# Optimization experiments

Measured on AMD Instinct MI355X. Metric: run time of the kernel, lower is better.

Reference implementation:

```python
import jax, jax.numpy as jnp
import numpy as np

N_EMBD = 512
Q_N_EMBD = 512
N_HEAD = 8
EPS = 1e-5


def _layernorm(x, w, b):
    mu = jnp.mean(x, axis=-1, keepdims=True)
    var = jnp.mean(jnp.square(x - mu), axis=-1, keepdims=True)
    return (x - mu) * jax.lax.rsqrt(var + EPS) * w + b


def setup_inputs() -> dict:
    key = jax.random.key(0)
    ks = jax.random.split(key, 16)
    B, C, H, W = 8, N_EMBD, 32, 32
    s = 1.0 / np.sqrt(N_EMBD)
    inp = {
        "q": jax.random.normal(ks[0], (B, Q_N_EMBD, H, W), jnp.float32),
        "kv": jax.random.normal(ks[1], (B, C, H, W), jnp.float32),
        "ln_kv_w": jnp.ones((N_EMBD,), jnp.float32),
        "ln_kv_b": jnp.zeros((N_EMBD,), jnp.float32),
        "ln_q_w": jnp.ones((Q_N_EMBD,), jnp.float32),
        "ln_q_b": jnp.zeros((Q_N_EMBD,), jnp.float32),
        "Wk": jax.random.normal(ks[2], (N_EMBD, N_EMBD), jnp.float32) * s,
        "bk": jnp.zeros((N_EMBD,), jnp.float32),
        "Wq": jax.random.normal(ks[3], (Q_N_EMBD, N_EMBD), jnp.float32) * s,
        "bq": jnp.zeros((N_EMBD,), jnp.float32),
        "Wv": jax.random.normal(ks[4], (N_EMBD, N_EMBD), jnp.float32) * s,
        "bv": jnp.zeros((N_EMBD,), jnp.float32),
        "Wp": jax.random.normal(ks[5], (N_EMBD, N_EMBD), jnp.float32) * s,
        "bp": jnp.zeros((N_EMBD,), jnp.float32),
    }
    return inp


def reference(q, kv, ln_kv_w, ln_kv_b, ln_q_w, ln_q_b,
              Wk, bk, Wq, bq, Wv, bv, Wp, bp):
    B, C, H, W = kv.shape
    c_q = q.shape[1]
    T = H * W
    hd = C // N_HEAD  # head dim

    # [B, C, H, W] -> [B, T, C] tokens
    kv_t = kv.reshape(B, C, T).transpose(0, 2, 1)
    q_t = q.reshape(B, c_q, T).transpose(0, 2, 1)

    kv_n = _layernorm(kv_t, ln_kv_w, ln_kv_b)
    q_n = _layernorm(q_t, ln_q_w, ln_q_b)

    # projections, split heads: [B, T, C] -> [B, H, T, hd]
    def heads(x):
        return x.reshape(B, T, N_HEAD, hd).transpose(0, 2, 1, 3)

    k = heads(kv_n @ Wk + bk)
    qh = heads(q_n @ Wq + bq)
    v = heads(kv_n @ Wv + bv)

    att = jnp.einsum('bhqd,bhkd->bhqk', qh, k) * (1.0 / np.sqrt(hd))
    att = jax.nn.softmax(att, axis=-1)
    y = jnp.einsum('bhqk,bhkd->bhqd', att, v)
    y = y.transpose(0, 2, 1, 3).reshape(B, T, C)
    y = y @ Wp + bp

    x = kv_t + y  # residual on (pre-LN) kv tokens
    return x.transpose(0, 2, 1).reshape(B, C, H, W)
```

## Files before the change

kernel.cpp:

```cpp
#include <hip/hip_runtime.h>
#include <stdint.h>

#define DI static __device__ __forceinline__

typedef __attribute__((ext_vector_type(8))) short bh8;
typedef __attribute__((ext_vector_type(4))) float f4;

DI short f2bf(float f) {
  unsigned u = __float_as_uint(f);
  u += 0x7fffu + ((u >> 16) & 1u);
  return (short)(u >> 16);
}

DI unsigned pkbf(float a, float b) {
  unsigned ua = __float_as_uint(a) + 0x8000u;
  unsigned ub = __float_as_uint(b) + 0x8000u;
  return __builtin_amdgcn_perm(ub, ua, 0x07060302u);
}

DI unsigned pk4fp8(float a, float b, float c, float d) {
  unsigned w = 0;
  w = __builtin_amdgcn_cvt_pk_fp8_f32(a, b, w, false);
  w = __builtin_amdgcn_cvt_pk_fp8_f32(c, d, w, true);
  return w;
}

DI void gll16(const void* g, void* l) {
  __builtin_amdgcn_global_load_lds(
      (const __attribute__((address_space(1))) unsigned int*)g,
      (__attribute__((address_space(3))) unsigned int*)l, 16, 0, 0);
}

DI f4 mfma16(bh8 a, bh8 b, f4 c) {
  return __builtin_amdgcn_mfma_f32_16x16x32_bf16(a, b, c, 0, 0, 0);
}

DI f4 mfma8(long a, long b, f4 c) {
  return __builtin_amdgcn_mfma_f32_16x16x32_fp8_fp8(a, b, c, 0, 0, 0);
}

DI bh8 ld8(const short* p) { return *(const bh8*)p; }

__global__ __launch_bounds__(256) void prep_k(
    const float* __restrict__ kv, const float* __restrict__ qi,
    const float* __restrict__ kw, const float* __restrict__ kbv,
    const float* __restrict__ qw, const float* __restrict__ qbv,
    const float* __restrict__ Wk, const float* __restrict__ Wq,
    const float* __restrict__ Wv, const float* __restrict__ Wp,
    short* __restrict__ kvn, short* __restrict__ qn,
    short* __restrict__ Wt)
{
  __shared__ char sm[16 * 516 * 4 + 128];
  int role = blockIdx.y;
  int bx = blockIdx.x;
  int tid = threadIdx.x;

  if (role < 4) {
    if (bx >= 256) return;
    float (*ts)[33] = (float(*)[33])sm;
    const float* w = (role == 0) ? Wk : (role == 1) ? Wq : (role == 2) ? Wv : Wp;
    short* o = Wt + ((size_t)role << 18);
    int c0 = (bx & 15) << 5, r0 = (bx >> 4) << 5;
    int tx = tid & 31, ty = tid >> 5;
#pragma unroll
    for (int k = 0; k < 32; k += 8)
      ts[ty + k][tx] = w[((size_t)(r0 + ty + k) << 9) + c0 + tx];
    __syncthreads();
#pragma unroll
    for (int k = 0; k < 32; k += 8)
      o[((size_t)(c0 + ty + k) << 9) + r0 + tx] = f2bf(ts[tx][ty + k]);
    return;
  }

  float (*xs)[516] = (float(*)[516])sm;
  float* smean = (float*)(sm + 16 * 516 * 4);
  float* srstd = smean + 16;
  int which = role - 4;
  const float* x = which ? qi : kv;
  const float* w = which ? qw : kw;
  const float* bb = which ? qbv : kbv;
  short* o = which ? qn : kvn;
  int b = bx >> 6;
  int t0 = (bx & 63) << 4;
  const float* xb = x + ((size_t)b << 19) + (size_t)t0;
#pragma unroll
  for (int k = 0; k < 8; k++) {
    int idx = (k << 8) + tid;
    int c = idx >> 2, tt = (idx & 3) << 2;
    float4 v = *(const float4*)(xb + ((size_t)c << 10) + tt);
    xs[tt + 0][c] = v.x; xs[tt + 1][c] = v.y;
    xs[tt + 2][c] = v.z; xs[tt + 3][c] = v.w;
  }
  __syncthreads();
  {
    int t = tid >> 4, cp = tid & 15;
    float s = 0.f, s2 = 0.f;
#pragma unroll
    for (int k = 0; k < 8; k++) {
      float4 v = *(const float4*)&xs[t][(cp << 2) + (k << 6)];
      s  += v.x + v.y + v.z + v.w;
      s2 += v.x * v.x + v.y * v.y + v.z * v.z + v.w * v.w;
    }
#pragma unroll
    for (int m = 1; m < 16; m <<= 1) {
      s  += __shfl_xor(s,  m);
      s2 += __shfl_xor(s2, m);
    }
    if (cp == 0) {
      float mean = s * (1.f / 512.f);
      float var  = s2 * (1.f / 512.f) - mean * mean;
      smean[t] = mean;
      srstd[t] = rsqrtf(var + 1e-5f);
    }
  }
  __syncthreads();
#pragma unroll
  for (int k = 0; k < 8; k++) {
    int idx = (k << 8) + tid;
    int t = idx >> 7, c = (idx & 127) << 2;
    float4 v = *(const float4*)&xs[t][c];
    float4 wv = *(const float4*)(w + c);
    float4 bv4 = *(const float4*)(bb + c);
    float mu = smean[t], rs = srstd[t];
    float r0 = (v.x - mu) * rs * wv.x + bv4.x;
    float r1 = (v.y - mu) * rs * wv.y + bv4.y;
    float r2 = (v.z - mu) * rs * wv.z + bv4.z;
    float r3 = (v.w - mu) * rs * wv.w + bv4.w;
    uint2 pk; pk.x = pkbf(r0, r1); pk.y = pkbf(r2, r3);
    *(uint2*)(o + (((size_t)(b << 10) + t0 + t) << 9) + c) = pk;
  }
}

__global__ __launch_bounds__(256, 3) void gemm_qkv_k(
    const short* __restrict__ kvn, const short* __restrict__ qn,
    const short* __restrict__ Wt,
    const float* __restrict__ bk, const float* __restrict__ bq,
    const float* __restrict__ bv,
    unsigned char* __restrict__ kb8, unsigned char* __restrict__ qb8,
    unsigned char* __restrict__ vb8)
{
  __shared__ short As[128 * 64];
  __shared__ short Bs[128 * 64];
  int z = blockIdx.z;
  const short* A; const short* Bt; const float* bias;
  int m0, n0;
  if (z == 0)      { A = Wt;             Bt = kvn;            bias = bk; }
  else if (z == 1) { A = Wt + (1 << 18); Bt = qn;             bias = bq; }
  else             { A = kvn;            Bt = Wt + (2 << 18); bias = bv; }
  if (z == 2) { m0 = blockIdx.x << 7; n0 = blockIdx.y << 7; }
  else        { m0 = blockIdx.y << 7; n0 = blockIdx.x << 7; }
  int tid = threadIdx.x;
  int lane = tid & 63, wid = tid >> 6;
  int r = lane & 15, g = lane >> 4;
  int wrow = (wid >> 1) << 6, wcol = (wid & 1) << 6;
  f4 acc[4][4];
#pragma unroll
  for (int i = 0; i < 4; i++)
#pragma unroll
    for (int j = 0; j < 4; j++) {
      acc[i][j][0] = 0.f; acc[i][j][1] = 0.f;
      acc[i][j][2] = 0.f; acc[i][j][3] = 0.f;
    }
  for (int k0 = 0; k0 < 512; k0 += 64) {
    __syncthreads();
#pragma unroll
    for (int it = 0; it < 4; it++) {
      int n = (it << 8) + tid;
      int row = n >> 3;
      int c = (n & 7) ^ (row & 7);
      gll16(A  + ((size_t)(m0 + row) << 9) + k0 + (c << 3), As + (n << 3));
      gll16(Bt + ((size_t)(n0 + row) << 9) + k0 + (c << 3), Bs + (n << 3));
    }
    __syncthreads();
    bh8 a[2][4], b[2][4];
#pragma unroll
    for (int ks = 0; ks < 2; ks++) {
#pragma unroll
      for (int i = 0; i < 4; i++) {
        int R = wrow + (i << 4) + r;
        a[ks][i] = ld8(As + (R << 6) + ((((ks << 2) + g) ^ (R & 7)) << 3));
      }
#pragma unroll
      for (int j = 0; j < 4; j++) {
        int R = wcol + (j << 4) + r;
        b[ks][j] = ld8(Bs + (R << 6) + ((((ks << 2) + g) ^ (R & 7)) << 3));
      }
    }
#pragma unroll
    for (int ks = 0; ks < 2; ks++)
#pragma unroll
      for (int i = 0; i < 4; i++)
#pragma unroll
        for (int j = 0; j < 4; j++)
          acc[i][j] = mfma16(a[ks][i], b[ks][j], acc[i][j]);
  }
#pragma unroll
  for (int i = 0; i < 4; i++) {
#pragma unroll
    for (int j = 0; j < 4; j++) {
      int mm = m0 + wrow + (i << 4) + (g << 2);
      int nn = n0 + wcol + (j << 4) + r;
      if (z == 0) {
        float4 b4 = *(const float4*)(bias + mm);
        int h = mm >> 6, d0 = mm & 63;
        int bb = nn >> 10, tt = nn & 1023;
        int c = tt & 255;
        int p = ((c & 15) << 4) | (c >> 4);
        size_t base = ((size_t)((bb * 8 + h) * 4 + (tt >> 8)) << 14);
        unsigned w = pk4fp8(acc[i][j][0] + b4.x, acc[i][j][1] + b4.y,
                            acc[i][j][2] + b4.z, acc[i][j][3] + b4.w);
        *(unsigned*)(kb8 + base + (p << 6) +
                     (((d0 >> 3) ^ (p & 7)) << 3) + (d0 & 7)) = w;
      } else if (z == 1) {
        float4 b4 = *(const float4*)(bias + mm);
        int h = mm >> 6, d0 = mm & 63;
        int bb = nn >> 10, tt = nn & 1023;
        unsigned w = pk4fp8(acc[i][j][0] + b4.x, acc[i][j][1] + b4.y,
                            acc[i][j][2] + b4.z, acc[i][j][3] + b4.w);
        *(unsigned*)(qb8 + ((((size_t)(bb * 8 + h)) << 10) + tt) * 64 + d0) = w;
      } else {
        float bvv = bias[nn];
        int h = nn >> 6, d = nn & 63;
        int bb = mm >> 10, tt = mm & 1023;
        int t8 = tt & 255;
        int tb = (((t8 >> 4) & 3) << 3) | (((t8 >> 3) & 1) << 2) | (t8 >> 6);
        size_t base = ((size_t)((bb * 8 + h) * 4 + (tt >> 8)) << 14);
        unsigned w = pk4fp8(acc[i][j][0] + bvv, acc[i][j][1] + bvv,
                            acc[i][j][2] + bvv, acc[i][j][3] + bvv);
        *(unsigned*)(vb8 + base + (d << 8) +
                     ((tb ^ (d & 31)) << 3) + (tt & 7)) = w;
      }
    }
  }
}

__global__ __launch_bounds__(256, 3) void gemm_proj_k(
    const short* __restrict__ A, const short* __restrict__ Bt,
    const float* __restrict__ bias, float* __restrict__ outp,
    const float* __restrict__ resid)
{
  __shared__ short As[64 * 64];
  __shared__ short Bs[128 * 64];
  int m0 = blockIdx.y << 6, n0 = blockIdx.x << 7;
  int tid = threadIdx.x;
  int lane = tid & 63, wid = tid >> 6;
  int r = lane & 15, g = lane >> 4;
  int wrow = (wid >> 1) << 5, wcol = (wid & 1) << 6;
  f4 acc[2][4];
#pragma unroll
  for (int i = 0; i < 2; i++)
#pragma unroll
    for (int j = 0; j < 4; j++) {
      acc[i][j][0] = 0.f; acc[i][j][1] = 0.f;
      acc[i][j][2] = 0.f; acc[i][j][3] = 0.f;
    }
  for (int k0 = 0; k0 < 512; k0 += 64) {
    __syncthreads();
#pragma unroll
    for (int it = 0; it < 2; it++) {
      int n = (it << 8) + tid;
      int row = n >> 3;
      int c = (n & 7) ^ (row & 7);
      gll16(A + ((size_t)(m0 + row) << 9) + k0 + (c << 3), As + (n << 3));
    }
#pragma unroll
    for (int it = 0; it < 4; it++) {
      int n = (it << 8) + tid;
      int row = n >> 3;
      int c = (n & 7) ^ (row & 7);
      gll16(Bt + ((size_t)(n0 + row) << 9) + k0 + (c << 3), Bs + (n << 3));
    }
    __syncthreads();
    bh8 a[2][2], b[2][4];
#pragma unroll
    for (int ks = 0; ks < 2; ks++) {
#pragma unroll
      for (int i = 0; i < 2; i++) {
        int R = wrow + (i << 4) + r;
        a[ks][i] = ld8(As + (R << 6) + ((((ks << 2) + g) ^ (R & 7)) << 3));
      }
#pragma unroll
      for (int j = 0; j < 4; j++) {
        int R = wcol + (j << 4) + r;
        b[ks][j] = ld8(Bs + (R << 6) + ((((ks << 2) + g) ^ (R & 7)) << 3));
      }
    }
#pragma unroll
    for (int ks = 0; ks < 2; ks++)
#pragma unroll
      for (int i = 0; i < 2; i++)
#pragma unroll
        for (int j = 0; j < 4; j++)
          acc[i][j] = mfma16(a[ks][i], b[ks][j], acc[i][j]);
  }
#pragma unroll
  for (int i = 0; i < 2; i++) {
#pragma unroll
    for (int j = 0; j < 4; j++) {
      int mm = m0 + wrow + (i << 4) + (g << 2);
      int nn = n0 + wcol + (j << 4) + r;
      int bb = nn >> 10, t = nn & 1023;
#pragma unroll
      for (int q = 0; q < 4; q++) {
        int m = mm + q;
        size_t ad = ((((size_t)bb << 9) + m) << 10) + t;
        outp[ad] = acc[i][j][q] + bias[m] + resid[ad];
      }
    }
  }
}

__global__ __launch_bounds__(256, 3) void attn_k(
    const unsigned char* __restrict__ qb8, const unsigned char* __restrict__ kb8,
    const unsigned char* __restrict__ vb8, short* __restrict__ yo)
{
  __shared__ char Ks[16384];
  __shared__ char Vs[16384];
  int h = blockIdx.x, b = blockIdx.z;
  int qt0 = blockIdx.y << 7;
  int tid = threadIdx.x, lane = tid & 63;
  int r = lane & 15, g = lane >> 4;
  int wbase = (tid >> 6) << 4;
  size_t bh = (size_t)(b * 8 + h);
  const unsigned char* Qg = qb8 + ((bh << 10) + qt0) * 64;
  const unsigned char* Kg = kb8 + (bh << 16);
  const unsigned char* Vg = vb8 + (bh << 16);

  long qf8[2][2];
#pragma unroll
  for (int u = 0; u < 2; u++)
#pragma unroll
    for (int ksd = 0; ksd < 2; ksd++)
      qf8[u][ksd] = *(const long*)(Qg +
          ((size_t)((u << 6) + wbase + r) << 6) + (((ksd << 2) + g) << 3));

  f4 oac[2][4];
#pragma unroll
  for (int u = 0; u < 2; u++)
#pragma unroll
    for (int jn = 0; jn < 4; jn++) {
      oac[u][jn][0] = 0.f; oac[u][jn][1] = 0.f;
      oac[u][jn][2] = 0.f; oac[u][jn][3] = 0.f;
    }
  float rs[2] = {0.f, 0.f};

  const float csc = 0.18033688011112042f;

  for (int ck = 0; ck < 4; ck++) {
    __syncthreads();
#pragma unroll
    for (int it = 0; it < 4; it++) {
      int n = ((it << 8) + tid) << 4;
      gll16(Kg + (ck << 14) + n, Ks + n);
      gll16(Vg + (ck << 14) + n, Vs + n);
    }
    __syncthreads();

    unsigned Wq2[2][4][4];
#pragma unroll
    for (int jq = 0; jq < 4; jq++) {
      f4 s2[2][4];
#pragma unroll
      for (int u = 0; u < 2; u++)
#pragma unroll
        for (int jj = 0; jj < 4; jj++) {
          s2[u][jj][0] = 0.f; s2[u][jj][1] = 0.f;
          s2[u][jj][2] = 0.f; s2[u][jj][3] = 0.f;
        }
#pragma unroll
      for (int ksd = 0; ksd < 2; ksd++)
#pragma unroll
        for (int jj = 0; jj < 4; jj++) {
          int j = (jq << 2) + jj;
          long kf = *(const long*)(Ks + (((j << 4) + r) << 6) +
                        ((((ksd << 2) + g) ^ (r & 7)) << 3));
          s2[0][jj] = mfma8(kf, qf8[0][ksd], s2[0][jj]);
          s2[1][jj] = mfma8(kf, qf8[1][ksd], s2[1][jj]);
        }
#pragma unroll
      for (int u = 0; u < 2; u++)
#pragma unroll
        for (int qq = 0; qq < 4; qq++) {
          float e0 = __builtin_amdgcn_exp2f(fminf(fmaf(s2[u][0][qq], csc, -3.0f), 8.5f));
          float e1 = __builtin_amdgcn_exp2f(fminf(fmaf(s2[u][1][qq], csc, -3.0f), 8.5f));
          float e2 = __builtin_amdgcn_exp2f(fminf(fmaf(s2[u][2][qq], csc, -3.0f), 8.5f));
          float e3 = __builtin_amdgcn_exp2f(fminf(fmaf(s2[u][3][qq], csc, -3.0f), 8.5f));
          rs[u] += (e0 + e1) + (e2 + e3);
          Wq2[u][qq][jq] = pk4fp8(e0, e1, e2, e3);
        }
    }

#pragma unroll
    for (int ks = 0; ks < 8; ks++) {
#pragma unroll
      for (int jn = 0; jn < 4; jn++) {
        int d = (jn << 4) + r;
        long bv8 = *(const long*)(Vs + (d << 8) +
                      ((((ks << 2) + g) ^ (d & 31)) << 3));
#pragma unroll
        for (int u = 0; u < 2; u++) {
          long ap = (long)(unsigned)Wq2[u][ks >> 1][(ks & 1) << 1] |
                    ((long)Wq2[u][ks >> 1][((ks & 1) << 1) + 1] << 32);
          oac[u][jn] = mfma8(ap, bv8, oac[u][jn]);
        }
      }
    }
  }

#pragma unroll
  for (int u = 0; u < 2; u++) {
    rs[u] += __shfl_xor(rs[u], 16);
    rs[u] += __shfl_xor(rs[u], 32);
  }

#pragma unroll
  for (int u = 0; u < 2; u++)
#pragma unroll
    for (int qq = 0; qq < 4; qq++) {
      float rsq = __shfl(rs[u], (g << 2) + qq);
      float inv = 1.f / (rsq + 1e-20f);
      int trow = qt0 + (u << 6) + wbase + (g << 2) + qq;
      size_t base = (((size_t)(b << 10) + trow) << 9) + (h << 6);
#pragma unroll
      for (int jn = 0; jn < 4; jn++)
        yo[base + (jn << 4) + r] = f2bf(oac[u][jn][qq] * inv);
    }
}

extern "C" void kernel_launch(void* const* d_in, const int* in_sizes, int n_in,
                              void* d_out, int out_size, void* d_ws, size_t ws_size,
                              hipStream_t stream)
{
  const float* q    = (const float*)d_in[0];
  const float* kv   = (const float*)d_in[1];
  const float* lnkw = (const float*)d_in[2];
  const float* lnkb = (const float*)d_in[3];
  const float* lnqw = (const float*)d_in[4];
  const float* lnqb = (const float*)d_in[5];
  const float* Wk   = (const float*)d_in[6];
  const float* bk   = (const float*)d_in[7];
  const float* Wq   = (const float*)d_in[8];
  const float* bq   = (const float*)d_in[9];
  const float* Wv   = (const float*)d_in[10];
  const float* bv   = (const float*)d_in[11];
  const float* Wp   = (const float*)d_in[12];
  const float* bp   = (const float*)d_in[13];

  char* ws = (char*)d_ws;
  const size_t SZ = (size_t)8192 * 512 * 2;
  short* buf0 = (short*)(ws);
  short* qn   = (short*)(ws + SZ);
  unsigned char* kb8 = (unsigned char*)(ws + 2 * SZ);
  unsigned char* qb8 = (unsigned char*)(ws + 3 * SZ);
  unsigned char* vb8 = (unsigned char*)(ws + 4 * SZ);
  short* Wt   = (short*)(ws + 5 * SZ);
  if (ws_size < 5 * SZ + 4 * 512 * 512 * 2) return;

  prep_k<<<dim3(512, 6), 256, 0, stream>>>(kv, q, lnkw, lnkb, lnqw, lnqb,
                                           Wk, Wq, Wv, Wp, buf0, qn, Wt);
  gemm_qkv_k<<<dim3(64, 4, 3), 256, 0, stream>>>(buf0, qn, Wt, bk, bq, bv,
                                                 kb8, qb8, vb8);
  attn_k<<<dim3(8, 8, 8), 256, 0, stream>>>(qb8, kb8, vb8, buf0);
  gemm_proj_k<<<dim3(64, 8), 256, 0, stream>>>(Wt + (3 << 18), buf0, bp,
                                               (float*)d_out, kv);
}
```

Baseline: 169.8 us.

## Fuse four kernels into one persistent megakernel with grid barriers

Replaces the four separate launches (prep, QKV GEMM, attention, projection) with a single persistent kernel of 768 blocks. The stages are separated by software grid barriers built on an atomic counter, which is cleared by a memset before launch. The goal is to remove the gaps and tail drain between kernel launches. In exchange it adds barrier spin costs and forces every stage onto a fixed block count and shared LDS size, and it relies on all 768 blocks being co-resident (3 per CU) to avoid deadlock.

```diff
diff --git a/kernel.cpp b/kernel.cpp
--- a/kernel.cpp
+++ b/kernel.cpp
@@ -2,6 +2,7 @@
 #include <stdint.h>
 
 #define DI static __device__ __forceinline__
+#define NB 768
 
 typedef __attribute__((ext_vector_type(8))) short bh8;
 typedef __attribute__((ext_vector_type(4))) float f4;
@@ -41,390 +42,412 @@
 
 DI bh8 ld8(const short* p) { return *(const bh8*)p; }
 
-__global__ __launch_bounds__(256) void prep_k(
+DI void gridbar(unsigned* c) {
+  __syncthreads();
+  if (threadIdx.x == 0) {
+    __threadfence();
+    atomicAdd(c, 1u);
+    while (__hip_atomic_load(c, __ATOMIC_RELAXED, __HIP_MEMORY_SCOPE_AGENT) < NB)
+      __builtin_amdgcn_s_sleep(2);
+    __threadfence();
+  }
+  __syncthreads();
+}
+
+__global__ __launch_bounds__(256, 3) void mega_k(
     const float* __restrict__ kv, const float* __restrict__ qi,
     const float* __restrict__ kw, const float* __restrict__ kbv,
     const float* __restrict__ qw, const float* __restrict__ qbv,
     const float* __restrict__ Wk, const float* __restrict__ Wq,
     const float* __restrict__ Wv, const float* __restrict__ Wp,
+    const float* __restrict__ bk, const float* __restrict__ bq,
+    const float* __restrict__ bv, const float* __restrict__ bp,
     short* __restrict__ kvn, short* __restrict__ qn,
-    short* __restrict__ Wt)
+    short* __restrict__ Wt,
+    unsigned char* __restrict__ kb8, unsigned char* __restrict__ qb8,
+    unsigned char* __restrict__ vb8,
+    short* __restrict__ yb, float* __restrict__ outp,
+    unsigned* __restrict__ bar)
 {
-  __shared__ char sm[16 * 516 * 4 + 128];
-  int role = blockIdx.y;
-  int bx = blockIdx.x;
+  __shared__ __align__(16) char SM[33280];
+  int bid = blockIdx.x;
   int tid = threadIdx.x;
 
-  if (role < 4) {
-    if (bx >= 256) return;
-    float (*ts)[33] = (float(*)[33])sm;
-    const float* w = (role == 0) ? Wk : (role == 1) ? Wq : (role == 2) ? Wv : Wp;
-    short* o = Wt + ((size_t)role << 18);
-    int c0 = (bx & 15) << 5, r0 = (bx >> 4) << 5;
-    int tx = tid & 31, ty = tid >> 5;
-#pragma unroll
-    for (int k = 0; k < 32; k += 8)
-      ts[ty + k][tx] = w[((size_t)(r0 + ty + k) << 9) + c0 + tx];
+  for (int k4 = 0; k4 < 4; k4++) {
+    int u = bid + k4 * NB;
+    int role = u >> 9;
+    int bx = u & 511;
     __syncthreads();
-#pragma unroll
-    for (int k = 0; k < 32; k += 8)
-      o[((size_t)(c0 + ty + k) << 9) + r0 + tx] = f2bf(ts[tx][ty + k]);
-    return;
-  }
-
-  float (*xs)[516] = (float(*)[516])sm;
-  float* smean = (float*)(sm + 16 * 516 * 4);
-  float* srstd = smean + 16;
-  int which = role - 4;
-  const float* x = which ? qi : kv;
-  const float* w = which ? qw : kw;
-  const float* bb = which ? qbv : kbv;
-  short* o = which ? qn : kvn;
-  int b = bx >> 6;
-  int t0 = (bx & 63) << 4;
-  const float* xb = x + ((size_t)b << 19) + (size_t)t0;
-#pragma unroll
-  for (int k = 0; k < 8; k++) {
-    int idx = (k << 8) + tid;
-    int c = idx >> 2, tt = (idx & 3) << 2;
-    float4 v = *(const float4*)(xb + ((size_t)c << 10) + tt);
-    xs[tt + 0][c] = v.x; xs[tt + 1][c] = v.y;
-    xs[tt + 2][c] = v.z; xs[tt + 3][c] = v.w;
-  }
-  __syncthreads();
-  {
-    int t = tid >> 4, cp = tid & 15;
-    float s = 0.f, s2 = 0.f;
-#pragma unroll
-    for (int k = 0; k < 8; k++) {
-      float4 v = *(const float4*)&xs[t][(cp << 2) + (k << 6)];
-      s  += v.x + v.y + v.z + v.w;
-      s2 += v.x * v.x + v.y * v.y + v.z * v.z + v.w * v.w;
-    }
-#pragma unroll
-    for (int m = 1; m < 16; m <<= 1) {
-      s  += __shfl_xor(s,  m);
-      s2 += __shfl_xor(s2, m);
-    }
-    if (cp == 0) {
-      float mean = s * (1.f / 512.f);
-      float var  = s2 * (1.f / 512.f) - mean * mean;
-      smean[t] = mean;
-      srstd[t] = rsqrtf(var + 1e-5f);
+    if (role < 4) {
+      if (bx < 256) {
+        float (*ts)[33] = (float(*)[33])SM;
+        const float* w = (role == 0) ? Wk : (role == 1) ? Wq
+                       : (role == 2) ? Wv : Wp;
+        short* o = Wt + ((size_t)role << 18);
+        int c0 = (bx & 15) << 5, r0 = (bx >> 4) << 5;
+        int tx = tid & 31, ty = tid >> 5;
+#pragma unroll
+        for (int k = 0; k < 32; k += 8)
+          ts[ty + k][tx] = w[((size_t)(r0 + ty + k) << 9) + c0 + tx];
+        __syncthreads();
+#pragma unroll
+        for (int k = 0; k < 32; k += 8)
+          o[((size_t)(c0 + ty + k) << 9) + r0 + tx] = f2bf(ts[tx][ty + k]);
+      }
+    } else {
+      float (*xs)[516] = (float(*)[516])SM;
+      float* smean = (float*)(SM + 16 * 516 * 4);
+      float* srstd = smean + 16;
+      int which = role - 4;
+      const float* x = which ? qi : kv;
+      const float* w = which ? qw : kw;
+      const float* bb = which ? qbv : kbv;
+      short* o = which ? qn : kvn;
+      int b = bx >> 6;
+      int t0 = (bx & 63) << 4;
+      const float* xb = x + ((size_t)b << 19) + (size_t)t0;
+#pragma unroll
+      for (int k = 0; k < 8; k++) {
+        int idx = (k << 8) + tid;
+        int c = idx >> 2, tt = (idx & 3) << 2;
+        float4 v = *(const float4*)(xb + ((size_t)c << 10) + tt);
+        xs[tt + 0][c] = v.x; xs[tt + 1][c] = v.y;
+        xs[tt + 2][c] = v.z; xs[tt + 3][c] = v.w;
+      }
+      __syncthreads();
+      {
+        int t = tid >> 4, cp = tid & 15;
+        float s = 0.f, s2 = 0.f;
+#pragma unroll
+        for (int k = 0; k < 8; k++) {
+          float4 v = *(const float4*)&xs[t][(cp << 2) + (k << 6)];
+          s  += v.x + v.y + v.z + v.w;
+          s2 += v.x * v.x + v.y * v.y + v.z * v.z + v.w * v.w;
+        }
+#pragma unroll
+        for (int m = 1; m < 16; m <<= 1) {
+          s  += __shfl_xor(s,  m);
+          s2 += __shfl_xor(s2, m);
+        }
+        if (cp == 0) {
+          float mean = s * (1.f / 512.f);
+          float var  = s2 * (1.f / 512.f) - mean * mean;
+          smean[t] = mean;
+          srstd[t] = rsqrtf(var + 1e-5f);
+        }
+      }
+      __syncthreads();
+#pragma unroll
+      for (int k = 0; k < 8; k++) {
+        int idx = (k << 8) + tid;
+        int t = idx >> 7, c = (idx & 127) << 2;
+        float4 v = *(const float4*)&xs[t][c];
+        float4 wv = *(const float4*)(w + c);
+        float4 bv4 = *(const float4*)(bb + c);
+        float mu = smean[t], rsd = srstd[t];
+        float r0 = (v.x - mu) * rsd * wv.x + bv4.x;
+        float r1 = (v.y - mu) * rsd * wv.y + bv4.y;
+        float r2 = (v.z - mu) * rsd * wv.z + bv4.z;
+        float r3 = (v.w - mu) * rsd * wv.w + bv4.w;
+        uint2 pk; pk.x = pkbf(r0, r1); pk.y = pkbf(r2, r3);
+        *(uint2*)(o + (((size_t)(b << 10) + t0 + t) << 9) + c) = pk;
+      }
     }
   }
-  __syncthreads();
-#pragma unroll
-  for (int k = 0; k < 8; k++) {
-    int idx = (k << 8) + tid;
-    int t = idx >> 7, c = (idx & 127) << 2;
-    float4 v = *(const float4*)&xs[t][c];
-    float4 wv = *(const float4*)(w + c);
-    float4 bv4 = *(const float4*)(bb + c);
-    float mu = smean[t], rs = srstd[t];
-    float r0 = (v.x - mu) * rs * wv.x + bv4.x;
-    float r1 = (v.y - mu) * rs * wv.y + bv4.y;
-    float r2 = (v.z - mu) * rs * wv.z + bv4.z;
-    float r3 = (v.w - mu) * rs * wv.w + bv4.w;
-    uint2 pk; pk.x = pkbf(r0, r1); pk.y = pkbf(r2, r3);
-    *(uint2*)(o + (((size_t)(b << 10) + t0 + t) << 9) + c) = pk;
-  }
-}
-
-__global__ __launch_bounds__(256, 3) void gemm_qkv_k(
-    const short* __restrict__ kvn, const short* __restrict__ qn,
-    const short* __restrict__ Wt,
-    const float* __restrict__ bk, const float* __restrict__ bq,
-    const float* __restrict__ bv,
-    unsigned char* __restrict__ kb8, unsigned char* __restrict__ qb8,
-    unsigned char* __restrict__ vb8)
-{
-  __shared__ short As[128 * 64];
-  __shared__ short Bs[128 * 64];
-  int z = blockIdx.z;
-  const short* A; const short* Bt; const float* bias;
-  int m0, n0;
-  if (z == 0)      { A = Wt;             Bt = kvn;            bias = bk; }
-  else if (z == 1) { A = Wt + (1 << 18); Bt = qn;             bias = bq; }
-  else             { A = kvn;            Bt = Wt + (2 << 18); bias = bv; }
-  if (z == 2) { m0 = blockIdx.x << 7; n0 = blockIdx.y << 7; }
-  else        { m0 = blockIdx.y << 7; n0 = blockIdx.x << 7; }
-  int tid = threadIdx.x;
-  int lane = tid & 63, wid = tid >> 6;
-  int r = lane & 15, g = lane >> 4;
-  int wrow = (wid >> 1) << 6, wcol = (wid & 1) << 6;
-  f4 acc[4][4];
-#pragma unroll
-  for (int i = 0; i < 4; i++)
-#pragma unroll
-    for (int j = 0; j < 4; j++) {
-      acc[i][j][0] = 0.f; acc[i][j][1] = 0.f;
-      acc[i][j][2] = 0.f; acc[i][j][3] = 0.f;
+  gridbar(bar + 0);
+
+  {
+    short* As = (short*)SM;
+    short* Bs = (short*)(SM + 16384);
+    int z = bid >> 8;
+    int rem = bid & 255;
+    int gy = rem >> 6, gx = rem & 63;
+    const short* A; const short* Bt; const float* bias;
+    int m0, n0;
+    if (z == 0)      { A = Wt;             Bt = kvn;            bias = bk; }
+    else if (z == 1) { A = Wt + (1 << 18); Bt = qn;             bias = bq; }
+    else             { A = kvn;            Bt = Wt + (2 << 18); bias = bv; }
+    if (z == 2) { m0 = gx << 7; n0 = gy << 7; }
+    else        { m0 = gy << 7; n0 = gx << 7; }
+    int lane = tid & 63, wid = tid >> 6;
+    int r = lane & 15, g = lane >> 4;
+    int wrow = (wid >> 1) << 6, wcol = (wid & 1) << 6;
+    f4 acc[4][4];
+#pragma unroll
+    for (int i = 0; i < 4; i++)
+#pragma unroll
+      for (int j = 0; j < 4; j++) {
+        acc[i][j][0] = 0.f; acc[i][j][1] = 0.f;
+        acc[i][j][2] = 0.f; acc[i][j][3] = 0.f;
+      }
+    for (int k0 = 0; k0 < 512; k0 += 64) {
+      __syncthreads();
+#pragma unroll
+      for (int it = 0; it < 4; it++) {
+        int n = (it << 8) + tid;
+        int row = n >> 3;
+        int c = (n & 7) ^ (row & 7);
+        gll16(A  + ((size_t)(m0 + row) << 9) + k0 + (c << 3), As + (n << 3));
+        gll16(Bt + ((size_t)(n0 + row) << 9) + k0 + (c << 3), Bs + (n << 3));
+      }
+      __syncthreads();
+      bh8 a[2][4], b[2][4];
+#pragma unroll
+      for (int ks = 0; ks < 2; ks++) {
+#pragma unroll
+        for (int i = 0; i < 4; i++) {
+          int R = wrow + (i << 4) + r;
+          a[ks][i] = ld8(As + (R << 6) + ((((ks << 2) + g) ^ (R & 7)) << 3));
+        }
+#pragma unroll
+        for (int j = 0; j < 4; j++) {
+          int R = wcol + (j << 4) + r;
+          b[ks][j] = ld8(Bs + (R << 6) + ((((ks << 2) + g) ^ (R & 7)) << 3));
+        }
+      }
+#pragma unroll
+      for (int ks = 0; ks < 2; ks++)
+#pragma unroll
+        for (int i = 0; i < 4; i++)
+#pragma unroll
+          for (int j = 0; j < 4; j++)
+            acc[i][j] = mfma16(a[ks][i], b[ks][j], acc[i][j]);
     }
-  for (int k0 = 0; k0 < 512; k0 += 64) {
-    __syncthreads();
-#pragma unroll
-    for (int it = 0; it < 4; it++) {
-      int n = (it << 8) + tid;
-      int row = n >> 3;
-      int c = (n & 7) ^ (row & 7);
-      gll16(A  + ((size_t)(m0 + row) << 9) + k0 + (c << 3), As + (n << 3));
-      gll16(Bt + ((size_t)(n0 + row) << 9) + k0 + (c << 3), Bs + (n << 3));
-    }
-    __syncthreads();
-    bh8 a[2][4], b[2][4];
-#pragma unroll
-    for (int ks = 0; ks < 2; ks++) {
-#pragma unroll
-      for (int i = 0; i < 4; i++) {
-        int R = wrow + (i << 4) + r;
-        a[ks][i] = ld8(As + (R << 6) + ((((ks << 2) + g) ^ (R & 7)) << 3));
-      }
+#pragma unroll
+    for (int i = 0; i < 4; i++) {
 #pragma unroll
       for (int j = 0; j < 4; j++) {
-        int R = wcol + (j << 4) + r;
-        b[ks][j] = ld8(Bs + (R << 6) + ((((ks << 2) + g) ^ (R & 7)) << 3));
-      }
-    }
-#pragma unroll
-    for (int ks = 0; ks < 2; ks++)
-#pragma unroll
-      for (int i = 0; i < 4; i++)
-#pragma unroll
-        for (int j = 0; j < 4; j++)
-          acc[i][j] = mfma16(a[ks][i], b[ks][j], acc[i][j]);
-  }
-#pragma unroll
-  for (int i = 0; i < 4; i++) {
-#pragma unroll
-    for (int j = 0; j < 4; j++) {
-      int mm = m0 + wrow + (i << 4) + (g << 2);
-      int nn = n0 + wcol + (j << 4) + r;
-      if (z == 0) {
-        float4 b4 = *(const float4*)(bias + mm);
-        int h = mm >> 6, d0 = mm & 63;
-        int bb = nn >> 10, tt = nn & 1023;
-        int c = tt & 255;
-        int p = ((c & 15) << 4) | (c >> 4);
-        size_t base = ((size_t)((bb * 8 + h) * 4 + (tt >> 8)) << 14);
-        unsigned w = pk4fp8(acc[i][j][0] + b4.x, acc[i][j][1] + b4.y,
-                            acc[i][j][2] + b4.z, acc[i][j][3] + b4.w);
-        *(unsigned*)(kb8 + base + (p << 6) +
-                     (((d0 >> 3) ^ (p & 7)) << 3) + (d0 & 7)) = w;
-      } else if (z == 1) {
-        float4 b4 = *(const float4*)(bias + mm);
-        int h = mm >> 6, d0 = mm & 63;
-        int bb = nn >> 10, tt = nn & 1023;
-        unsigned w = pk4fp8(acc[i][j][0] + b4.x, acc[i][j][1] + b4.y,
-                            acc[i][j][2] + b4.z, acc[i][j][3] + b4.w);
-        *(unsigned*)(qb8 + ((((size_t)(bb * 8 + h)) << 10) + tt) * 64 + d0) = w;
-      } else {
-        float bvv = bias[nn];
-        int h = nn >> 6, d = nn & 63;
-        int bb = mm >> 10, tt = mm & 1023;
-        int t8 = tt & 255;
-        int tb = (((t8 >> 4) & 3) << 3) | (((t8 >> 3) & 1) << 2) | (t8 >> 6);
-        size_t base = ((size_t)((bb * 8 + h) * 4 + (tt >> 8)) << 14);
-        unsigned w = pk4fp8(acc[i][j][0] + bvv, acc[i][j][1] + bvv,
-                            acc[i][j][2] + bvv, acc[i][j][3] + bvv);
-        *(unsigned*)(vb8 + base + (d << 8) +
-                     ((tb ^ (d & 31)) << 3) + (tt & 7)) = w;
+        int mm = m0 + wrow + (i << 4) + (g << 2);
+        int nn = n0 + wcol + (j << 4) + r;
+        if (z == 0) {
+          float4 b4 = *(const float4*)(bias + mm);
+          int h = mm >> 6, d0 = mm & 63;
+          int bb = nn >> 10, tt = nn & 1023;
+          int c = tt & 255;
+          int p = ((c & 15) << 4) | (c >> 4);
+          size_t base = ((size_t)((bb * 8 + h) * 4 + (tt >> 8)) << 14);
+          unsigned w = pk4fp8(acc[i][j][0] + b4.x, acc[i][j][1] + b4.y,
+                              acc[i][j][2] + b4.z, acc[i][j][3] + b4.w);
+          *(unsigned*)(kb8 + base + (p << 6) +
+                       (((d0 >> 3) ^ (p & 7)) << 3) + (d0 & 7)) = w;
+        } else if (z == 1) {
+          float4 b4 = *(const float4*)(bias + mm);
+          int h = mm >> 6, d0 = mm & 63;
+          int bb = nn >> 10, tt = nn & 1023;
+          unsigned w = pk4fp8(acc[i][j][0] + b4.x, acc[i][j][1] + b4.y,
+                              acc[i][j][2] + b4.z, acc[i][j][3] + b4.w);
+          *(unsigned*)(qb8 + ((((size_t)(bb * 8 + h)) << 10) + tt) * 64 + d0) = w;
+        } else {
+          float bvv = bias[nn];
+          int h = nn >> 6, d = nn & 63;
+          int bb = mm >> 10, tt = mm & 1023;
+          int t8 = tt & 255;
+          int tb = (((t8 >> 4) & 3) << 3) | (((t8 >> 3) & 1) << 2) | (t8 >> 6);
+          size_t base = ((size_t)((bb * 8 + h) * 4 + (tt >> 8)) << 14);
+          unsigned w = pk4fp8(acc[i][j][0] + bvv, acc[i][j][1] + bvv,
+                              acc[i][j][2] + bvv, acc[i][j][3] + bvv);
+          *(unsigned*)(vb8 + base + (d << 8) +
+                       ((tb ^ (d & 31)) << 3) + (tt & 7)) = w;
+        }
       }
     }
   }
-}
-
-__global__ __launch_bounds__(256, 3) void gemm_proj_k(
-    const short* __restrict__ A, const short* __restrict__ Bt,
-    const float* __restrict__ bias, float* __restrict__ outp,
-    const float* __restrict__ resid)
-{
-  __shared__ short As[64 * 64];
-  __shared__ short Bs[128 * 64];
-  int m0 = blockIdx.y << 6, n0 = blockIdx.x << 7;
-  int tid = threadIdx.x;
-  int lane = tid & 63, wid = tid >> 6;
-  int r = lane & 15, g = lane >> 4;
-  int wrow = (wid >> 1) << 5, wcol = (wid & 1) << 6;
-  f4 acc[2][4];
-#pragma unroll
-  for (int i = 0; i < 2; i++)
-#pragma unroll
-    for (int j = 0; j < 4; j++) {
-      acc[i][j][0] = 0.f; acc[i][j][1] = 0.f;
-      acc[i][j][2] = 0.f; acc[i][j][3] = 0.f;
-    }
-  for (int k0 = 0; k0 < 512; k0 += 64) {
-    __syncthreads();
-#pragma unroll
-    for (int it = 0; it < 2; it++) {
-      int n = (it << 8) + tid;
-      int row = n >> 3;
-      int c = (n & 7) ^ (row & 7);
-      gll16(A + ((size_t)(m0 + row) << 9) + k0 + (c << 3), As + (n << 3));
-    }
-#pragma unroll
-    for (int it = 0; it < 4; it++) {
-      int n = (it << 8) + tid;
-      int row = n >> 3;
-      int c = (n & 7) ^ (row & 7);
-      gll16(Bt + ((size_t)(n0 + row) << 9) + k0 + (c << 3), Bs + (n << 3));
-    }
-    __syncthreads();
-    bh8 a[2][2], b[2][4];
-#pragma unroll
-    for (int ks = 0; ks < 2; ks++) {
-#pragma unroll
-      for (int i = 0; i < 2; i++) {
-        int R = wrow + (i << 4) + r;
-        a[ks][i] = ld8(As + (R << 6) + ((((ks << 2) + g) ^ (R & 7)) << 3));
-      }
-#pragma unroll
-      for (int j = 0; j < 4; j++) {
-        int R = wcol + (j << 4) + r;
-        b[ks][j] = ld8(Bs + (R << 6) + ((((ks << 2) + g) ^ (R & 7)) << 3));
-      }
-    }
-#pragma unroll
-    for (int ks = 0; ks < 2; ks++)
-#pragma unroll
-      for (int i = 0; i < 2; i++)
-#pragma unroll
-        for (int j = 0; j < 4; j++)
-          acc[i][j] = mfma16(a[ks][i], b[ks][j], acc[i][j]);
-  }
-#pragma unroll
-  for (int i = 0; i < 2; i++) {
-#pragma unroll
-    for (int j = 0; j < 4; j++) {
-      int mm = m0 + wrow + (i << 4) + (g << 2);
-      int nn = n0 + wcol + (j << 4) + r;
-      int bb = nn >> 10, t = nn & 1023;
-#pragma unroll
-      for (int q = 0; q < 4; q++) {
-        int m = mm + q;
-        size_t ad = ((((size_t)bb << 9) + m) << 10) + t;
-        outp[ad] = acc[i][j][q] + bias[m] + resid[ad];
-      }
+  gridbar(bar + 1);
+
+  {
+    int m3 = bid % 3;
+    if (m3 < 2) {
+      int u = (bid / 3) * 2 + m3;
+      char* Ks = SM;
+      char* Vs = SM + 16384;
+      int h = u & 7, yq = (u >> 3) & 7, b = u >> 6;
+      int qt0 = yq << 7;
+      int lane = tid & 63;
+      int r = lane & 15, g = lane >> 4;
+      int wbase = (tid >> 6) << 4;
+      size_t bh = (size_t)(b * 8 + h);
+      const unsigned char* Qg = qb8 + ((bh << 10) + qt0) * 64;
+      const unsigned char* Kg = kb8 + (bh << 16);
+      const unsigned char* Vg = vb8 + (bh << 16);
+
+      long qf8[2][2];
+#pragma unroll
+      for (int uu = 0; uu < 2; uu++)
+#pragma unroll
+        for (int ksd = 0; ksd < 2; ksd++)
+          qf8[uu][ksd] = *(const long*)(Qg +
+              ((size_t)((uu << 6) + wbase + r) << 6) + (((ksd << 2) + g) << 3));
+
+      f4 oac[2][4];
+#pragma unroll
+      for (int uu = 0; uu < 2; uu++)
+#pragma unroll
+        for (int jn = 0; jn < 4; jn++) {
+          oac[uu][jn][0] = 0.f; oac[uu][jn][1] = 0.f;
+          oac[uu][jn][2] = 0.f; oac[uu][jn][3] = 0.f;
+        }
+      float rsm[2] = {0.f, 0.f};
+
+      const float csc = 0.18033688011112042f;
+
+      for (int ck = 0; ck < 4; ck++) {
+        __syncthreads();
+#pragma unroll
+        for (int it = 0; it < 4; it++) {
+          int n = ((it << 8) + tid) << 4;
+          gll16(Kg + (ck << 14) + n, Ks + n);
+          gll16(Vg + (ck << 14) + n, Vs + n);
+        }
+        __syncthreads();
+
+        unsigned Wq2[2][4][4];
+#pragma unroll
+        for (int jq = 0; jq < 4; jq++) {
+          f4 s2[2][4];
+#pragma unroll
+          for (int uu = 0; uu < 2; uu++)
+#pragma unroll
+            for (int jj = 0; jj < 4; jj++) {
+              s2[uu][jj][0] = 0.f; s2[uu][jj][1] = 0.f;
+              s2[uu][jj][2] = 0.f; s2[uu][jj][3] = 0.f;
+            }
+#pragma unroll
+          for (int ksd = 0; ksd < 2; ksd++)
+#pragma unroll
+            for (int jj = 0; jj < 4; jj++) {
+              int j = (jq << 2) + jj;
+              long kf = *(const long*)(Ks + (((j << 4) + r) << 6) +
+                            ((((ksd << 2) + g) ^ (r & 7)) << 3));
+              s2[0][jj] = mfma8(kf, qf8[0][ksd], s2[0][jj]);
+              s2[1][jj] = mfma8(kf, qf8[1][ksd], s2[1][jj]);
+            }
+#pragma unroll
+          for (int uu = 0; uu < 2; uu++)
+#pragma unroll
+            for (int qq = 0; qq < 4; qq++) {
+              float e0 = __builtin_amdgcn_exp2f(fminf(fmaf(s2[uu][0][qq], csc, -3.0f), 8.5f));
+              float e1 = __builtin_amdgcn_exp2f(fminf(fmaf(s2[uu][1][qq], csc, -3.0f), 8.5f));
+              float e2 = __builtin_amdgcn_exp2f(fminf(fmaf(s2[uu][2][qq], csc, -3.0f), 8.5f));
+              float e3 = __builtin_amdgcn_exp2f(fminf(fmaf(s2[uu][3][qq], csc, -3.0f), 8.5f));
+              rsm[uu] += (e0 + e1) + (e2 + e3);
+              Wq2[uu][qq][jq] = pk4fp8(e0, e1, e2, e3);
+            }
+        }
+
+#pragma unroll
+        for (int ks = 0; ks < 8; ks++) {
+#pragma unroll
+          for (int jn = 0; jn < 4; jn++) {
+            int d = (jn << 4) + r;
+            long bv8 = *(const long*)(Vs + (d << 8) +
+                          ((((ks << 2) + g) ^ (d & 31)) << 3));
+#pragma unroll
+            for (int uu = 0; uu < 2; uu++) {
+              long ap = (long)(unsigned)Wq2[uu][ks >> 1][(ks & 1) << 1] |
+                        ((long)Wq2[uu][ks >> 1][((ks & 1) << 1) + 1] << 32);
+              oac[uu][jn] = mfma8(ap, bv8, oac[uu][jn]);
+            }
+          }
+        }
+      }
+
+#pragma unroll
+      for (int uu = 0; uu < 2; uu++) {
+        rsm[uu] += __shfl_xor(rsm[uu], 16);
+        rsm[uu] += __shfl_xor(rsm[uu], 32);
+      }
+#pragma unroll
+      for (int uu = 0; uu < 2; uu++)
+#pragma unroll
+        for (int qq = 0; qq < 4; qq++) {
+          float rsq = __shfl(rsm[uu], (g << 2) + qq);
+          float inv = 1.f / (rsq + 1e-20f);
+          int trow = qt0 + (uu << 6) + wbase + (g << 2) + qq;
+          size_t base = (((size_t)(b << 10) + trow) << 9) + (h << 6);
+#pragma unroll
+          for (int jn = 0; jn < 4; jn++)
+            yb[base + (jn << 4) + r] = f2bf(oac[uu][jn][qq] * inv);
+        }
     }
   }
-}
-
-__global__ __launch_bounds__(256, 3) void attn_k(
-    const unsigned char* __restrict__ qb8, const unsigned char* __restrict__ kb8,
-    const unsigned char* __restrict__ vb8, short* __restrict__ yo)
-{
-  __shared__ char Ks[16384];
-  __shared__ char Vs[16384];
-  int h = blockIdx.x, b = blockIdx.z;
-  int qt0 = blockIdx.y << 7;
-  int tid = threadIdx.x, lane = tid & 63;
-  int r = lane & 15, g = lane >> 4;
-  int wbase = (tid >> 6) << 4;
-  size_t bh = (size_t)(b * 8 + h);
-  const unsigned char* Qg = qb8 + ((bh << 10) + qt0) * 64;
-  const unsigned char* Kg = kb8 + (bh << 16);
-  const unsigned char* Vg = vb8 + (bh << 16);
-
-  long qf8[2][2];
-#pragma unroll
-  for (int u = 0; u < 2; u++)
-#pragma unroll
-    for (int ksd = 0; ksd < 2; ksd++)
-      qf8[u][ksd] = *(const long*)(Qg +
-          ((size_t)((u << 6) + wbase + r) << 6) + (((ksd << 2) + g) << 3));
-
-  f4 oac[2][4];
-#pragma unroll
-  for (int u = 0; u < 2; u++)
-#pragma unroll
-    for (int jn = 0; jn < 4; jn++) {
-      oac[u][jn][0] = 0.f; oac[u][jn][1] = 0.f;
-      oac[u][jn][2] = 0.f; oac[u][jn][3] = 0.f;
-    }
-  float rs[2] = {0.f, 0.f};
-
-  const float csc = 0.18033688011112042f;
-
-  for (int ck = 0; ck < 4; ck++) {
-    __syncthreads();
-#pragma unroll
-    for (int it = 0; it < 4; it++) {
-      int n = ((it << 8) + tid) << 4;
-      gll16(Kg + (ck << 14) + n, Ks + n);
-      gll16(Vg + (ck << 14) + n, Vs + n);
-    }
-    __syncthreads();
-
-    unsigned Wq2[2][4][4];
-#pragma unroll
-    for (int jq = 0; jq < 4; jq++) {
-      f4 s2[2][4];
-#pragma unroll
-      for (int u = 0; u < 2; u++)
-#pragma unroll
-        for (int jj = 0; jj < 4; jj++) {
-          s2[u][jj][0] = 0.f; s2[u][jj][1] = 0.f;
-          s2[u][jj][2] = 0.f; s2[u][jj][3] = 0.f;
-        }
-#pragma unroll
-      for (int ksd = 0; ksd < 2; ksd++)
-#pragma unroll
-        for (int jj = 0; jj < 4; jj++) {
-          int j = (jq << 2) + jj;
-          long kf = *(const long*)(Ks + (((j << 4) + r) << 6) +
-                        ((((ksd << 2) + g) ^ (r & 7)) << 3));
-          s2[0][jj] = mfma8(kf, qf8[0][ksd], s2[0][jj]);
-          s2[1][jj] = mfma8(kf, qf8[1][ksd], s2[1][jj]);
-        }
-#pragma unroll
-      for (int u = 0; u < 2; u++)
-#pragma unroll
-        for (int qq = 0; qq < 4; qq++) {
-          float e0 = __builtin_amdgcn_exp2f(fminf(fmaf(s2[u][0][qq], csc, -3.0f), 8.5f));
-          float e1 = __builtin_amdgcn_exp2f(fminf(fmaf(s2[u][1][qq], csc, -3.0f), 8.5f));
-          float e2 = __builtin_amdgcn_exp2f(fminf(fmaf(s2[u][2][qq], csc, -3.0f), 8.5f));
-          float e3 = __builtin_amdgcn_exp2f(fminf(fmaf(s2[u][3][qq], csc, -3.0f), 8.5f));
-          rs[u] += (e0 + e1) + (e2 + e3);
-          Wq2[u][qq][jq] = pk4fp8(e0, e1, e2, e3);
-        }
-    }
-
-#pragma unroll
-    for (int ks = 0; ks < 8; ks++) {
-#pragma unroll
-      for (int jn = 0; jn < 4; jn++) {
-        int d = (jn << 4) + r;
-        long bv8 = *(const long*)(Vs + (d << 8) +
-                      ((((ks << 2) + g) ^ (d & 31)) << 3));
-#pragma unroll
-        for (int u = 0; u < 2; u++) {
-          long ap = (long)(unsigned)Wq2[u][ks >> 1][(ks & 1) << 1] |
-                    ((long)Wq2[u][ks >> 1][((ks & 1) << 1) + 1] << 32);
-          oac[u][jn] = mfma8(ap, bv8, oac[u][jn]);
+  gridbar(bar + 2);
+
+  {
+    int m3 = bid % 3;
+    if (m3 < 2) {
+      int u = (bid / 3) * 2 + m3;
+      short* As = (short*)SM;
+      short* Bs = (short*)(SM + 8192);
+      const short* A = Wt + (3 << 18);
+      const short* Bt = yb;
+      int m0 = (u >> 6) << 6, n0 = (u & 63) << 7;
+      int lane = tid & 63, wid = tid >> 6;
+      int r = lane & 15, g = lane >> 4;
+      int wrow = (wid >> 1) << 5, wcol = (wid & 1) << 6;
+      f4 acc[2][4];
+#pragma unroll
+      for (int i = 0; i < 2; i++)
+#pragma unroll
+        for (int j = 0; j < 4; j++) {
+          acc[i][j][0] = 0.f; acc[i][j][1] = 0.f;
+          acc[i][j][2] = 0.f; acc[i][j][3] = 0.f;
+        }
+      for (int k0 = 0; k0 < 512; k0 += 64) {
+        __syncthreads();
+#pragma unroll
+        for (int it = 0; it < 2; it++) {
+          int n = (it << 8) + tid;
+          int row = n >> 3;
+          int c = (n & 7) ^ (row & 7);
+          gll16(A + ((size_t)(m0 + row) << 9) + k0 + (c << 3), As + (n << 3));
+        }
+#pragma unroll
+        for (int it = 0; it < 4; it++) {
+          int n = (it << 8) + tid;
+          int row = n >> 3;
+          int c = (n & 7) ^ (row & 7);
+          gll16(Bt + ((size_t)(n0 + row) << 9) + k0 + (c << 3), Bs + (n << 3));
+        }
+        __syncthreads();
+        bh8 a[2][2], b[2][4];
+#pragma unroll
+        for (int ks = 0; ks < 2; ks++) {
+#pragma unroll
+          for (int i = 0; i < 2; i++) {
+            int R = wrow + (i << 4) + r;
+            a[ks][i] = ld8(As + (R << 6) + ((((ks << 2) + g) ^ (R & 7)) << 3));
+          }
+#pragma unroll
+          for (int j = 0; j < 4; j++) {
+            int R = wcol + (j << 4) + r;
+            b[ks][j] = ld8(Bs + (R << 6) + ((((ks << 2) + g) ^ (R & 7)) << 3));
+          }
+        }
+#pragma unroll
+        for (int ks = 0; ks < 2; ks++)
+#pragma unroll
+          for (int i = 0; i < 2; i++)
+#pragma unroll
+            for (int j = 0; j < 4; j++)
+              acc[i][j] = mfma16(a[ks][i], b[ks][j], acc[i][j]);
+      }
+#pragma unroll
+      for (int i = 0; i < 2; i++) {
+#pragma unroll
+        for (int j = 0; j < 4; j++) {
+          int mm = m0 + wrow + (i << 4) + (g << 2);
+          int nn = n0 + wcol + (j << 4) + r;
+          int bb = nn >> 10, t = nn & 1023;
+#pragma unroll
+          for (int q = 0; q < 4; q++) {
+            int m = mm + q;
+            size_t ad = ((((size_t)bb << 9) + m) << 10) + t;
+            outp[ad] = acc[i][j][q] + bp[m] + kv[ad];
+          }
         }
       }
     }
   }
-
-#pragma unroll
-  for (int u = 0; u < 2; u++) {
-    rs[u] += __shfl_xor(rs[u], 16);
-    rs[u] += __shfl_xor(rs[u], 32);
-  }
-
-#pragma unroll
-  for (int u = 0; u < 2; u++)
-#pragma unroll
-    for (int qq = 0; qq < 4; qq++) {
-      float rsq = __shfl(rs[u], (g << 2) + qq);
-      float inv = 1.f / (rsq + 1e-20f);
-      int trow = qt0 + (u << 6) + wbase + (g << 2) + qq;
-      size_t base = (((size_t)(b << 10) + trow) << 9) + (h << 6);
-#pragma unroll
-      for (int jn = 0; jn < 4; jn++)
-        yo[base + (jn << 4) + r] = f2bf(oac[u][jn][qq] * inv);
-    }
 }
 
 extern "C" void kernel_launch(void* const* d_in, const int* in_sizes, int n_in,
@@ -448,19 +471,19 @@
 
   char* ws = (char*)d_ws;
   const size_t SZ = (size_t)8192 * 512 * 2;
-  short* buf0 = (short*)(ws);
+  short* kvn  = (short*)(ws);
   short* qn   = (short*)(ws + SZ);
   unsigned char* kb8 = (unsigned char*)(ws + 2 * SZ);
   unsigned char* qb8 = (unsigned char*)(ws + 3 * SZ);
   unsigned char* vb8 = (unsigned char*)(ws + 4 * SZ);
   short* Wt   = (short*)(ws + 5 * SZ);
-  if (ws_size < 5 * SZ + 4 * 512 * 512 * 2) return;
-
-  prep_k<<<dim3(512, 6), 256, 0, stream>>>(kv, q, lnkw, lnkb, lnqw, lnqb,
-                                           Wk, Wq, Wv, Wp, buf0, qn, Wt);
-  gemm_qkv_k<<<dim3(64, 4, 3), 256, 0, stream>>>(buf0, qn, Wt, bk, bq, bv,
-                                                 kb8, qb8, vb8);
-  attn_k<<<dim3(8, 8, 8), 256, 0, stream>>>(qb8, kb8, vb8, buf0);
-  gemm_proj_k<<<dim3(64, 8), 256, 0, stream>>>(Wt + (3 << 18), buf0, bp,
-                                               (float*)d_out, kv);
-}
+  short* yb   = (short*)(ws + 6 * SZ);
+  unsigned* bar = (unsigned*)(ws + 7 * SZ);
+  if (ws_size < 7 * SZ + 256) return;
+
+  hipMemsetAsync(bar, 0, 256, stream);
+  mega_k<<<dim3(NB), dim3(256), 0, stream>>>(
+      kv, q, lnkw, lnkb, lnqw, lnqb, Wk, Wq, Wv, Wp,
+      bk, bq, bv, bp, kvn, qn, Wt, kb8, qb8, vb8,
+      yb, (float*)d_out, bar);
+}
```

After: 461.9 us. 2.72x slower.
